# Optimization experiments

Measured on AMD Instinct MI355X. Metric: run time of the kernel, lower is better.

## Reference

```python
import jax, jax.numpy as jnp
import numpy as np

B, NQ, L, E, K = 64, 1024, 128, 8192, 2
LN_EPS = 1e-5


def setup_inputs() -> dict:
    key = jax.random.key(0)
    ks = jax.random.split(key, 16)
    s1 = 1.0 / np.sqrt(2 * L + 1)
    s2 = 1.0 / np.sqrt(L)
    s3 = 1.0 / np.sqrt(2 * L)
    return {
        "z0": jax.random.normal(ks[0], (B, L), jnp.float32),
        "edge_index": jax.random.randint(ks[1], (2, E), 0, NQ, jnp.int64),
        "edge_attr": jax.random.normal(ks[2], (E,), jnp.float32),
        "n_qubits": NQ,
        # edge MLP params, stacked over K message-passing rounds
        "e_w1": jax.random.normal(ks[3], (K, L, 2 * L + 1), jnp.float32) * s1,
        "e_b1": jnp.zeros((K, L), jnp.float32),
        "e_w2": jax.random.normal(ks[4], (K, L, L), jnp.float32) * s2,
        "e_b2": jnp.zeros((K, L), jnp.float32),
        # node MLP params
        "n_w1": jax.random.normal(ks[5], (K, L, 2 * L), jnp.float32) * s3,
        "n_b1": jnp.zeros((K, L), jnp.float32),
        "ln_g": jnp.ones((K, L), jnp.float32),
        "ln_b": jnp.zeros((K, L), jnp.float32),
        "n_w2": jax.random.normal(ks[6], (K, L, L), jnp.float32) * s2,
        "n_b2": jnp.zeros((K, L), jnp.float32),
    }


def reference(z0, edge_index, edge_attr, n_qubits,
              e_w1, e_b1, e_w2, e_b2,
              n_w1, n_b1, ln_g, ln_b, n_w2, n_b2):
    b, l = z0.shape
    src, tgt = edge_index[0], edge_index[1]
    e_ = src.shape[0]
    # broadcast latent z0 to every node: h [B, N, L]
    h = jnp.broadcast_to(z0[:, None, :], (b, n_qubits, l))
    e = jnp.broadcast_to(edge_attr[None, :, None], (b, e_, 1))  # [B, E, 1]
    k_rounds = e_w1.shape[0]
    for k in range(k_rounds):
        hi = h[:, src, :]  # gather source node feats [B, E, L]
        hj = h[:, tgt, :]  # gather target node feats [B, E, L]
        inp_e = jnp.concatenate([hi, hj, e], axis=-1)  # [B, E, 2L+1]
        m = jax.nn.relu(inp_e @ e_w1[k].T + e_b1[k]) @ e_w2[k].T + e_b2[k]
        # scatter_add messages back to source nodes
        m_agg = jnp.zeros_like(h).at[:, src, :].add(m)
        inp_n = jnp.concatenate([h, m_agg], axis=-1)  # [B, N, 2L]
        x = jax.nn.relu(inp_n @ n_w1[k].T + n_b1[k])
        mu = x.mean(axis=-1, keepdims=True)
        var = ((x - mu) ** 2).mean(axis=-1, keepdims=True)
        x = (x - mu) * jax.lax.rsqrt(var + LN_EPS) * ln_g[k] + ln_b[k]
        # Dropout(p=0.1) is identity in eval mode
        h = x @ n_w2[k].T + n_b2[k] + h  # residual
    return h.mean(axis=1)  # [B, L]
```

## Files before the change

### kernel.cpp

```cpp
#include <hip/hip_runtime.h>

#define B_   64
#define NQ_  1024
#define L_   128
#define E_   8192
#define M_   (B_*NQ_)
#define LDP  136

typedef unsigned short u16;
typedef unsigned int   u32;
typedef __attribute__((ext_vector_type(8))) short short8;
typedef __attribute__((ext_vector_type(4))) float floatx4;

#define WVB() __builtin_amdgcn_wave_barrier()

__device__ __forceinline__ u16 f2bf(float f) {
    union { float f; u32 u; } v; v.f = f;
    return (u16)((v.u + 0x7fffu + ((v.u >> 16) & 1u)) >> 16);
}
__device__ __forceinline__ float bf2f(u16 u) {
    union { u32 u; float f; } v; v.u = ((u32)u) << 16;
    return v.f;
}
__device__ __forceinline__ floatx4 mfma16(short8 a, short8 b, floatx4 c) {
    return __builtin_amdgcn_mfma_f32_16x16x32_bf16(a, b, c, 0, 0, 0);
}
__device__ __forceinline__ short8 gfrag(const u16* base, int r0, int kb, int lane) {
    return *(const short8*)(base + (size_t)(r0 + (lane & 15)) * 128 + kb * 32 + (lane >> 4) * 8);
}
__device__ __forceinline__ short8 sfrag(const u16* t, int r0, int kb, int lane) {
    return *(const short8*)(t + (r0 + (lane & 15)) * LDP + kb * 32 + (lane >> 4) * 8);
}
__device__ __forceinline__ short8 frag_cvt(const float* base, int r0, int ld, int kb, int lane) {
    const float* p = base + (size_t)(r0 + (lane & 15)) * ld + kb * 32 + (lane >> 4) * 8;
    short8 s;
#pragma unroll
    for (int j = 0; j < 8; ++j) s[j] = (short)f2bf(p[j]);
    return s;
}
__device__ __forceinline__ void tile_store(u16* t, const floatx4* acc, int lane) {
    int col = lane & 15, qd = lane >> 4;
#pragma unroll
    for (int nt = 0; nt < 8; ++nt)
#pragma unroll
        for (int r = 0; r < 4; ++r)
            t[(qd * 4 + r) * LDP + nt * 16 + col] = f2bf(acc[nt][r]);
}
__device__ __forceinline__ void tile_flush(const u16* t, u16* g, int lane) {
#pragma unroll
    for (int it = 0; it < 4; ++it) {
        int chunk = it * 64 + lane, row = chunk >> 4, c8 = chunk & 15;
        *(uint4*)(g + (size_t)row * 128 + c8 * 8) = *(const uint4*)(t + row * LDP + c8 * 8);
    }
}
__device__ __forceinline__ void stage_w(u16* wbuf, const u16* g, int tid) {
    const uint4* g4 = (const uint4*)g;
#pragma unroll
    for (int i = 0; i < 8; ++i) {
        int idx = tid + i * 256, row = idx >> 4, c8 = idx & 15;
        *(uint4*)&wbuf[row * LDP + c8 * 8] = g4[idx];
    }
}

__global__ __launch_bounds__(256) void k_setup(const int* __restrict__ ei,
                                               const float* __restrict__ attr,
                                               const float* __restrict__ z0,
                                               const float* __restrict__ e_w1,
                                               const float* __restrict__ e_b1,
                                               const float* __restrict__ e_w2,
                                               const float* __restrict__ e_b2,
                                               const float* __restrict__ n_w1,
                                               const float* __restrict__ n_b1,
                                               const float* __restrict__ n_w2,
                                               const float* __restrict__ n_b2,
                                               int* __restrict__ ofs,
                                               int* __restrict__ tgt_s,
                                               float* __restrict__ a_s,
                                               float* __restrict__ degf,
                                               u16* __restrict__ wb,
                                               float* __restrict__ wl,
                                               float* __restrict__ vb2,
                                               float* __restrict__ rx,
                                               float* __restrict__ rci,
                                               float* __restrict__ rcj,
                                               float* __restrict__ rh,
                                               float* __restrict__ mx0,
                                               u16* __restrict__ c0t) {
    __shared__ __align__(16) char smem[52608];
    int tid = threadIdx.x, blk = blockIdx.x;
    int lane = tid & 63, w = tid >> 6, col = lane & 15, qd = lane >> 4;

    if (blk == 0) {
        int* cnt  = (int*)smem;
        int* wsum = cnt + 1024;
        int* flag = wsum + 8;
#pragma unroll
        for (int i = 0; i < 4; ++i) cnt[tid + i * 256] = 0;
        if (tid == 0) *flag = 1;
        __syncthreads();
        if (tid < 100 && ei[2 * tid + 1] != 0) atomicAnd(flag, 0);
        __syncthreads();
        int i64 = *flag;
        for (int e = tid; e < E_; e += 256) {
            int s = i64 ? ei[2 * e] : ei[e];
            atomicAdd(&cnt[s], 1);
        }
        __syncthreads();
        int q0 = tid * 4;
        int c0 = cnt[q0], c1 = cnt[q0 + 1], c2 = cnt[q0 + 2], c3 = cnt[q0 + 3];
        int tsum = c0 + c1 + c2 + c3, incl = tsum;
#pragma unroll
        for (int o = 1; o < 64; o <<= 1) {
            int t = __shfl_up(incl, o, 64);
            if (lane >= o) incl += t;
        }
        if (lane == 63) wsum[w] = incl;
        __syncthreads();
        int wo = 0;
        for (int i = 0; i < w; ++i) wo += wsum[i];
        int base = wo + incl - tsum;
        ofs[q0] = base; ofs[q0 + 1] = base + c0;
        ofs[q0 + 2] = base + c0 + c1; ofs[q0 + 3] = base + c0 + c1 + c2;
        degf[q0] = (float)c0; degf[q0 + 1] = (float)c1;
        degf[q0 + 2] = (float)c2; degf[q0 + 3] = (float)c3;
        if (tid == 0) ofs[NQ_] = E_;
        __syncthreads();
        cnt[q0] = base; cnt[q0 + 1] = base + c0;
        cnt[q0 + 2] = base + c0 + c1; cnt[q0 + 3] = base + c0 + c1 + c2;
        __syncthreads();
        for (int e = tid; e < E_; e += 256) {
            int s = i64 ? ei[2 * e]        : ei[e];
            int t = i64 ? ei[2 * (E_ + e)] : ei[E_ + e];
            int pos = atomicAdd(&cnt[s], 1);
            tgt_s[pos] = t;
            a_s[pos]   = attr[e];
        }
    } else if (blk <= 2) {
        const float* src = (blk == 1) ? n_w2 : (n_w2 + 16384);
        u16* dst = wb + ((blk == 1) ? 1 : 6) * 16384;
        for (int idx = tid; idx < 16384; idx += 256) dst[idx] = f2bf(src[idx]);
    } else if (blk <= 7) {
        const float* P; const float* Q; int ldp; u16* D;
        switch (blk) {
            case 3: P = n_w1 + 128;             ldp = 256; Q = e_w2;         D = wb;             break;
            case 4: P = n_w1 + 32768 + 128;     ldp = 256; Q = e_w2 + 16384; D = wb + 5 * 16384; break;
            case 5: P = e_w1 + 128 * 257;       ldp = 257; Q = n_w2;         D = wb + 2 * 16384; break;
            case 6: P = e_w1 + 128 * 257 + 128; ldp = 257; Q = n_w2;         D = wb + 3 * 16384; break;
            default:P = n_w1 + 32768;           ldp = 256; Q = n_w2;         D = wb + 4 * 16384; break;
        }
        u16* qt = (u16*)smem;
        u16* tl = (u16*)(smem + 34816);
        for (int idx = tid; idx < 16384; idx += 256) {
            int c = idx >> 7, kd = idx & 127;
            qt[kd * LDP + c] = f2bf(Q[idx]);
        }
        __syncthreads();
        for (int t = 0; t < 2; ++t) {
            int r0 = (w * 2 + t) * 16;
            floatx4 acc[8] = {};
#pragma unroll
            for (int kb = 0; kb < 4; ++kb) {
                short8 a = frag_cvt(P, r0, ldp, kb, lane);
#pragma unroll
                for (int nt = 0; nt < 8; ++nt)
                    acc[nt] = mfma16(a, sfrag(qt, nt * 16, kb, lane), acc[nt]);
            }
            u16* slot = tl + w * 16 * LDP;
            tile_store(slot, acc, lane); WVB();
            tile_flush(slot, D + (size_t)r0 * 128, lane); WVB();
        }
    } else if (blk == 8) {
        int r0 = w * 16;
        floatx4 acc[8] = {};
#pragma unroll
        for (int kb = 0; kb < 4; ++kb) {
            short8 a = frag_cvt(z0, r0, 128, kb, lane);
#pragma unroll
            for (int nt = 0; nt < 8; ++nt)
                acc[nt] = mfma16(a, frag_cvt(n_w1, nt * 16, 256, kb, lane), acc[nt]);
        }
#pragma unroll
        for (int nt = 0; nt < 8; ++nt) {
            int cg = nt * 16 + col; float bv = n_b1[cg];
#pragma unroll
            for (int r = 0; r < 4; ++r) rx[(r0 + qd * 4 + r) * 128 + cg] = acc[nt][r] + bv;
        }
    } else if (blk <= 11) {
        int r0 = w * 16;
        const float* Wp; int ld; const float* bias; float* dst;
        if (blk == 9)       { Wp = e_w1 + 128 * 257;       ld = 257; bias = e_b1 + 128; dst = rci; }
        else if (blk == 10) { Wp = e_w1 + 128 * 257 + 128; ld = 257; bias = nullptr;    dst = rcj; }
        else                { Wp = n_w1 + 32768;           ld = 256; bias = n_b1 + 128; dst = rh;  }
        floatx4 acc[8] = {};
#pragma unroll
        for (int kb = 0; kb < 4; ++kb) {
            short8 a;
            int rr = (r0 + (lane & 15)) * 128, kk = kb * 32 + (lane >> 4) * 8;
#pragma unroll
            for (int j = 0; j < 8; ++j) a[j] = (short)f2bf(z0[rr + kk + j] + n_b2[kk + j]);
#pragma unroll
            for (int nt = 0; nt < 8; ++nt)
                acc[nt] = mfma16(a, frag_cvt(Wp, nt * 16, ld, kb, lane), acc[nt]);
        }
#pragma unroll
        for (int nt = 0; nt < 8; ++nt) {
            int cg = nt * 16 + col;
            float bv = bias ? bias[cg] : 0.0f;
#pragma unroll
            for (int r = 0; r < 4; ++r) dst[(r0 + qd * 4 + r) * 128 + cg] = acc[nt][r] + bv;
        }
    } else if (blk == 12) {
        u16* tl = (u16*)(smem + 34816);
        int r0 = w * 16;
        floatx4 a1[8] = {};
#pragma unroll
        for (int kb = 0; kb < 4; ++kb) {
            short8 a = frag_cvt(z0, r0, 128, kb, lane);
#pragma unroll
            for (int nt = 0; nt < 8; ++nt) {
                a1[nt] = mfma16(a, frag_cvt(e_w1,       nt * 16, 257, kb, lane), a1[nt]);
                a1[nt] = mfma16(a, frag_cvt(e_w1 + 128, nt * 16, 257, kb, lane), a1[nt]);
            }
        }
#pragma unroll
        for (int nt = 0; nt < 8; ++nt) {
            float bv = e_b1[nt * 16 + col];
#pragma unroll
            for (int r = 0; r < 4; ++r) a1[nt][r] += bv;
        }
        u16* slot = tl + w * 16 * LDP;
        tile_store(slot, a1, lane); WVB();
        tile_flush(slot, c0t + (size_t)r0 * 128, lane);
    } else {
        int k = tid >> 7, c = tid & 127;
        float s = 0.0f;
        for (int n = 0; n < 128; ++n)
            s += n_w1[k * 32768 + c * 256 + 128 + n] * e_b2[k * 128 + n];
        vb2[tid] = s;
        wl[tid]  = e_w1[k * 128 * 257 + c * 257 + 256];
        for (int i = tid; i < 8192; i += 256) mx0[i] = 0.0f;
    }
}

template <bool R0>
__global__ __launch_bounds__(256) void k_edge(const u16* __restrict__ ci,
                                              const u16* __restrict__ cj,
                                              const int* __restrict__ ofs,
                                              const int* __restrict__ tgt_s,
                                              const float* __restrict__ a_s,
                                              const float* __restrict__ wl,
                                              u16* __restrict__ S) {
    int tid = threadIdx.x, lane = tid & 63, w = tid >> 6;
    int gw = blockIdx.x * 4 + w;
    int q = gw & (NQ_ - 1), bg = gw >> 10;
    int bl[8];
#pragma unroll
    for (int i = 0; i < 4; ++i) { bl[i] = bg * 4 + i; bl[i + 4] = bg * 4 + i + 32; }
    float2 wl2 = ((const float2*)wl)[lane];
    int st = ofs[q], en = ofs[q + 1];
    float ax[8] = {}, ay[8] = {};
    if (R0) {
        float cx[8], cy[8];
#pragma unroll
        for (int i = 0; i < 8; ++i) {
            u32 cv = ((const u32*)ci)[(size_t)bl[i] * 64 + lane];
            cx[i] = bf2f((u16)(cv & 0xffff)); cy[i] = bf2f((u16)(cv >> 16));
        }
        for (int idx = st; idx < en; ++idx) {
            float a = a_s[idx];
            float wx = a * wl2.x, wy = a * wl2.y;
#pragma unroll
            for (int i = 0; i < 8; ++i) {
                ax[i] += fmaxf(cx[i] + wx, 0.f);
                ay[i] += fmaxf(cy[i] + wy, 0.f);
            }
        }
    } else {
        const u32* cjp[8];
        float cx[8], cy[8];
#pragma unroll
        for (int i = 0; i < 8; ++i) {
            cjp[i] = (const u32*)cj + (size_t)bl[i] * NQ_ * 64;
            u32 cv = ((const u32*)ci)[((size_t)bl[i] * NQ_ + q) * 64 + lane];
            cx[i] = bf2f((u16)(cv & 0xffff)); cy[i] = bf2f((u16)(cv >> 16));
        }
        for (int idx = st; idx < en; ++idx) {
            int t = tgt_s[idx];
            float a = a_s[idx];
            size_t ro = (size_t)t * 64 + lane;
            float wx = a * wl2.x, wy = a * wl2.y;
#pragma unroll
            for (int i = 0; i < 8; ++i) {
                u32 jv = cjp[i][ro];
                ax[i] += fmaxf(cx[i] + bf2f((u16)(jv & 0xffff)) + wx, 0.f);
                ay[i] += fmaxf(cy[i] + bf2f((u16)(jv >> 16))    + wy, 0.f);
            }
        }
    }
    u32* Sp = (u32*)S;
#pragma unroll
    for (int i = 0; i < 8; ++i)
        Sp[((size_t)bl[i] * NQ_ + q) * 64 + lane] =
            (u32)f2bf(ax[i]) | ((u32)f2bf(ay[i]) << 16);
}

__global__ __launch_bounds__(256, 2) void k_node0(const u16* __restrict__ S,
                                                  const u16* __restrict__ wb,
                                                  const float* __restrict__ rx,
                                                  const float* __restrict__ vb2,
                                                  const float* __restrict__ degf,
                                                  const float* __restrict__ rci,
                                                  const float* __restrict__ rcj,
                                                  const float* __restrict__ rh,
                                                  const float* __restrict__ g,
                                                  const float* __restrict__ bb,
                                                  float* __restrict__ mx0,
                                                  u16* __restrict__ t1,
                                                  u16* __restrict__ ci1,
                                                  u16* __restrict__ cj1) {
    __shared__ u16 wbuf[128 * LDP];
    __shared__ u16 xt[8][16 * LDP];
    __shared__ float rsum[4][128];
    int tid = threadIdx.x, lane = tid & 63, w = tid >> 6;
    int col = lane & 15, qd = lane >> 4;
    int rowbase = blockIdx.x * 128 + w * 32;
    int b = blockIdx.x >> 3;

    stage_w(wbuf, wb, tid);
    __syncthreads();
    floatx4 xa[2][8] = {};
#pragma unroll
    for (int kb = 0; kb < 4; ++kb) {
        short8 Bv[8];
#pragma unroll
        for (int nt = 0; nt < 8; ++nt) Bv[nt] = sfrag(wbuf, nt * 16, kb, lane);
#pragma unroll
        for (int t = 0; t < 2; ++t) {
            short8 a = gfrag(S, rowbase + t * 16, kb, lane);
#pragma unroll
            for (int nt = 0; nt < 8; ++nt) xa[t][nt] = mfma16(a, Bv[nt], xa[t][nt]);
        }
    }
    float s8[8] = {};
#pragma unroll
    for (int t = 0; t < 2; ++t) {
#pragma unroll
        for (int nt = 0; nt < 8; ++nt) {
            int cg = nt * 16 + col;
            float base = rx[b * 128 + cg], vb = vb2[cg];
#pragma unroll
            for (int r = 0; r < 4; ++r) {
                int row = rowbase + t * 16 + qd * 4 + r;
                xa[t][nt][r] = fmaxf(xa[t][nt][r] + base + degf[row & (NQ_ - 1)] * vb, 0.f);
            }
        }
#pragma unroll
        for (int r = 0; r < 4; ++r) {
            float s = 0.f, s2 = 0.f;
#pragma unroll
            for (int nt = 0; nt < 8; ++nt) { float v = xa[t][nt][r]; s += v; s2 += v * v; }
#pragma unroll
            for (int o = 1; o < 16; o <<= 1) { s += __shfl_xor(s, o, 64); s2 += __shfl_xor(s2, o, 64); }
            float mu = s * (1.f / 128.f), var = s2 * (1.f / 128.f) - mu * mu;
            float rs = rsqrtf(var + 1e-5f);
#pragma unroll
            for (int nt = 0; nt < 8; ++nt) {
                int cg = nt * 16 + col;
                float xv = (xa[t][nt][r] - mu) * rs * g[cg] + bb[cg];
                xa[t][nt][r] = xv;
                s8[nt] += xv;
            }
        }
        tile_store(&xt[w * 2 + t][0], xa[t], lane);
    }
#pragma unroll
    for (int nt = 0; nt < 8; ++nt) {
        s8[nt] += __shfl_xor(s8[nt], 16, 64);
        s8[nt] += __shfl_xor(s8[nt], 32, 64);
    }
    if (lane < 16) {
#pragma unroll
        for (int nt = 0; nt < 8; ++nt) rsum[w][nt * 16 + lane] = s8[nt];
    }
    __syncthreads();
    if (tid < 128) {
        float v = rsum[0][tid] + rsum[1][tid] + rsum[2][tid] + rsum[3][tid];
        atomicAdd(mx0 + b * 128 + tid, v);
    }

#pragma unroll
    for (int ph = 0; ph < 3; ++ph) {
        const u16* Wsl = wb + ((ph == 0) ? 4 : (ph == 1) ? 2 : 3) * 16384;
        const float* rt = (ph == 0) ? rh : (ph == 1) ? rci : rcj;
        u16* dstg = (ph == 0) ? t1 : (ph == 1) ? ci1 : cj1;
        __syncthreads();
        stage_w(wbuf, Wsl, tid);
        __syncthreads();
        floatx4 ca[2][8] = {};
#pragma unroll
        for (int kb = 0; kb < 4; ++kb) {
            short8 Bv[8];
#pragma unroll
            for (int nt = 0; nt < 8; ++nt) Bv[nt] = sfrag(wbuf, nt * 16, kb, lane);
#pragma unroll
            for (int t = 0; t < 2; ++t) {
                short8 a = sfrag(&xt[w * 2 + t][0], 0, kb, lane);
#pragma unroll
                for (int nt = 0; nt < 8; ++nt) ca[t][nt] = mfma16(a, Bv[nt], ca[t][nt]);
            }
        }
#pragma unroll
        for (int t = 0; t < 2; ++t)
#pragma unroll
            for (int nt = 0; nt < 8; ++nt) {
                float rc = rt[b * 128 + nt * 16 + col];
#pragma unroll
                for (int r = 0; r < 4; ++r) ca[t][nt][r] += rc;
            }
        __syncthreads();
#pragma unroll
        for (int t = 0; t < 2; ++t) tile_store(wbuf + (w * 2 + t) * 16 * LDP, ca[t], lane);
        WVB();
#pragma unroll
        for (int t = 0; t < 2; ++t)
            tile_flush(wbuf + (w * 2 + t) * 16 * LDP, dstg + (size_t)(rowbase + t * 16) * 128, lane);
    }
}

__global__ __launch_bounds__(256, 2) void k_node1(const u16* __restrict__ S,
                                                  const u16* __restrict__ t1,
                                                  const u16* __restrict__ wb,
                                                  const float* __restrict__ vb2,
                                                  const float* __restrict__ degf,
                                                  const float* __restrict__ g,
                                                  const float* __restrict__ bb,
                                                  const float* __restrict__ z0,
                                                  const float* __restrict__ n_b2,
                                                  const float* __restrict__ mx0,
                                                  float* __restrict__ out) {
    __shared__ u16 wbuf[128 * LDP];
    __shared__ u16 xt[8][16 * LDP];
    __shared__ float rsum[4][128];
    int tid = threadIdx.x, lane = tid & 63, w = tid >> 6;
    int col = lane & 15, qd = lane >> 4;
    int rowbase = blockIdx.x * 128 + w * 32;
    int b = blockIdx.x >> 3;

    stage_w(wbuf, wb + 5 * 16384, tid);
    __syncthreads();
    floatx4 xa[2][8] = {};
#pragma unroll
    for (int kb = 0; kb < 4; ++kb) {
        short8 Bv[8];
#pragma unroll
        for (int nt = 0; nt < 8; ++nt) Bv[nt] = sfrag(wbuf, nt * 16, kb, lane);
#pragma unroll
        for (int t = 0; t < 2; ++t) {
            short8 a = gfrag(S, rowbase + t * 16, kb, lane);
#pragma unroll
            for (int nt = 0; nt < 8; ++nt) xa[t][nt] = mfma16(a, Bv[nt], xa[t][nt]);
        }
    }
#pragma unroll
    for (int t = 0; t < 2; ++t) {
#pragma unroll
        for (int nt = 0; nt < 8; ++nt) {
            int cg = nt * 16 + col;
            float vb = vb2[cg];
#pragma unroll
            for (int r = 0; r < 4; ++r) {
                int row = rowbase + t * 16 + qd * 4 + r;
                float tv = bf2f(t1[(size_t)row * 128 + cg]);
                xa[t][nt][r] = fmaxf(xa[t][nt][r] + tv + degf[row & (NQ_ - 1)] * vb, 0.f);
            }
        }
#pragma unroll
        for (int r = 0; r < 4; ++r) {
            float s = 0.f, s2 = 0.f;
#pragma unroll
            for (int nt = 0; nt < 8; ++nt) { float v = xa[t][nt][r]; s += v; s2 += v * v; }
#pragma unroll
            for (int o = 1; o < 16; o <<= 1) { s += __shfl_xor(s, o, 64); s2 += __shfl_xor(s2, o, 64); }
            float mu = s * (1.f / 128.f), var = s2 * (1.f / 128.f) - mu * mu;
            float rs = rsqrtf(var + 1e-5f);
#pragma unroll
            for (int nt = 0; nt < 8; ++nt) {
                int cg = nt * 16 + col;
                xa[t][nt][r] = (xa[t][nt][r] - mu) * rs * g[cg] + bb[cg];
            }
        }
        tile_store(&xt[w * 2 + t][0], xa[t], lane);
    }
    __syncthreads();

    stage_w(wbuf, wb + 6 * 16384, tid);
    __syncthreads();
    floatx4 ma[2][8] = {};
#pragma unroll
    for (int kb = 0; kb < 4; ++kb) {
        short8 Bv[8];
#pragma unroll
        for (int nt = 0; nt < 8; ++nt) Bv[nt] = sfrag(wbuf, nt * 16, kb, lane);
#pragma unroll
        for (int t = 0; t < 2; ++t) {
            short8 a = sfrag(&xt[w * 2 + t][0], 0, kb, lane);
#pragma unroll
            for (int nt = 0; nt < 8; ++nt) ma[t][nt] = mfma16(a, Bv[nt], ma[t][nt]);
        }
    }
    float s8[8] = {};
#pragma unroll
    for (int t = 0; t < 2; ++t)
#pragma unroll
        for (int nt = 0; nt < 8; ++nt)
#pragma unroll
            for (int r = 0; r < 4; ++r) s8[nt] += ma[t][nt][r];
#pragma unroll
    for (int nt = 0; nt < 8; ++nt) {
        s8[nt] += __shfl_xor(s8[nt], 16, 64);
        s8[nt] += __shfl_xor(s8[nt], 32, 64);
    }
    if (lane < 16) {
#pragma unroll
        for (int nt = 0; nt < 8; ++nt) rsum[w][nt * 16 + lane] = s8[nt];
    }
    __syncthreads();
    if (tid < 128) {
        float v = rsum[0][tid] + rsum[1][tid] + rsum[2][tid] + rsum[3][tid];
        atomicAdd(out + b * 128 + tid, v * (1.f / 1024.f));
    }

    if ((blockIdx.x & 7) == 0 && tid < 128) {
        int c = tid;
        const u16* w2s = wb + 1 * 16384;
        const float* mx = mx0 + b * 128;
        float s = 0.f;
#pragma unroll 4
        for (int k = 0; k < 128; ++k) s += mx[k] * bf2f(w2s[c * 128 + k]);
        float acc = z0[b * 128 + c] + n_b2[c] + n_b2[128 + c] + s * (1.f / 1024.f);
        atomicAdd(out + b * 128 + c, acc);
    }
}

extern "C" void kernel_launch(void* const* d_in, const int* in_sizes, int n_in,
                              void* d_out, int out_size, void* d_ws, size_t ws_size,
                              hipStream_t stream) {
    const float* z0   = (const float*)d_in[0];
    const int*   ei   = (const int*)d_in[1];
    const float* attr = (const float*)d_in[2];
    const float* e_w1 = (const float*)d_in[4];
    const float* e_b1 = (const float*)d_in[5];
    const float* e_w2 = (const float*)d_in[6];
    const float* e_b2 = (const float*)d_in[7];
    const float* n_w1 = (const float*)d_in[8];
    const float* n_b1 = (const float*)d_in[9];
    const float* ln_g = (const float*)d_in[10];
    const float* ln_b = (const float*)d_in[11];
    const float* n_w2 = (const float*)d_in[12];
    const float* n_b2 = (const float*)d_in[13];
    float* out = (float*)d_out;

    const size_t H = (size_t)M_ * L_;
    float* f     = (float*)d_ws;
    float* degf  = f;
    float* a_s   = f + 1024;
    float* wl    = a_s + 8192;
    float* vb2   = wl + 256;
    float* rx    = vb2 + 256;
    float* rci   = rx + 8192;
    float* rcj   = rci + 8192;
    float* rh    = rcj + 8192;
    float* mx0   = rh + 8192;
    int*   ofs   = (int*)(mx0 + 8192);
    int*   tgt_s = ofs + 1056;
    u16*   wb    = (u16*)(tgt_s + 8192);
    u16*   c0t   = wb + 7 * 16384;
    u16*   S     = c0t + 8192;
    u16*   t1    = S + H;
    u16*   ci1   = t1 + H;
    u16*   cj1   = ci1 + H;

    hipMemsetAsync(out, 0, 8192 * sizeof(float), stream);

    k_setup<<<14, 256, 0, stream>>>(ei, attr, z0, e_w1, e_b1, e_w2, e_b2,
                                    n_w1, n_b1, n_w2, n_b2,
                                    ofs, tgt_s, a_s, degf, wb, wl, vb2,
                                    rx, rci, rcj, rh, mx0, c0t);

    k_edge<true><<<2048, 256, 0, stream>>>(c0t, nullptr, ofs, tgt_s, a_s, wl, S);

    k_node0<<<512, 256, 0, stream>>>(S, wb, rx, vb2, degf, rci, rcj, rh,
                                     ln_g, ln_b, mx0, t1, ci1, cj1);

    k_edge<false><<<2048, 256, 0, stream>>>(ci1, cj1, ofs, tgt_s, a_s, wl + 128, S);

    k_node1<<<512, 256, 0, stream>>>(S, t1, wb, vb2 + 128, degf,
                                     ln_g + 128, ln_b + 128, z0, n_b2, mx0, out);
}
```

Before: 190.9 us.

## Store weights in MFMA fragment order and read them directly from global

Setup now writes the folded bf16 weight matrices in a per-lane MFMA fragment layout. The node kernels load B fragments straight from global or L2 with coalesced 16-byte reads instead of staging the whole 128x128 weight into LDS behind a block barrier. Node1 also runs its second GEMM per wave through a small LDS tile and sends per-wave atomics to the output, which drops the block-wide barriers and the rsum reduction. The trade-off is repeated global or L2 weight reads per wave and four times as many atomics, in exchange for less LDS, fewer syncs and possibly higher occupancy.

New measurement: 192.4 us. No clear change (+0.8%).

```diff
diff --git a/kernel.cpp b/kernel.cpp
--- a/kernel.cpp
+++ b/kernel.cpp
@@ -6,6 +6,7 @@
 #define E_   8192
 #define M_   (B_*NQ_)
 #define LDP  136
+#define TILE 2176
 
 typedef unsigned short u16;
 typedef unsigned int   u32;
@@ -31,6 +32,14 @@
 __device__ __forceinline__ short8 sfrag(const u16* t, int r0, int kb, int lane) {
     return *(const short8*)(t + (r0 + (lane & 15)) * LDP + kb * 32 + (lane >> 4) * 8);
 }
+__device__ __forceinline__ short8 wfrag(const u16* wf, int nt, int kb, int lane) {
+    return *(const short8*)(wf + (((kb << 3) + nt) * 64 + lane) * 8);
+}
+__device__ __forceinline__ void frag_flush(const u16* t, u16* wf, int nt, int lane) {
+#pragma unroll
+    for (int kb = 0; kb < 4; ++kb)
+        *(short8*)(wf + (((kb << 3) + nt) * 64 + lane) * 8) = sfrag(t, 0, kb, lane);
+}
 __device__ __forceinline__ short8 frag_cvt(const float* base, int r0, int ld, int kb, int lane) {
     const float* p = base + (size_t)(r0 + (lane & 15)) * ld + kb * 32 + (lane >> 4) * 8;
     short8 s;
@@ -53,40 +62,23 @@
         *(uint4*)(g + (size_t)row * 128 + c8 * 8) = *(const uint4*)(t + row * LDP + c8 * 8);
     }
 }
-__device__ __forceinline__ void stage_w(u16* wbuf, const u16* g, int tid) {
-    const uint4* g4 = (const uint4*)g;
-#pragma unroll
-    for (int i = 0; i < 8; ++i) {
-        int idx = tid + i * 256, row = idx >> 4, c8 = idx & 15;
-        *(uint4*)&wbuf[row * LDP + c8 * 8] = g4[idx];
-    }
-}
-
-__global__ __launch_bounds__(256) void k_setup(const int* __restrict__ ei,
-                                               const float* __restrict__ attr,
-                                               const float* __restrict__ z0,
-                                               const float* __restrict__ e_w1,
-                                               const float* __restrict__ e_b1,
-                                               const float* __restrict__ e_w2,
-                                               const float* __restrict__ e_b2,
-                                               const float* __restrict__ n_w1,
-                                               const float* __restrict__ n_b1,
-                                               const float* __restrict__ n_w2,
-                                               const float* __restrict__ n_b2,
-                                               int* __restrict__ ofs,
-                                               int* __restrict__ tgt_s,
-                                               float* __restrict__ a_s,
-                                               float* __restrict__ degf,
-                                               u16* __restrict__ wb,
-                                               float* __restrict__ wl,
-                                               float* __restrict__ vb2,
-                                               float* __restrict__ rx,
-                                               float* __restrict__ rci,
-                                               float* __restrict__ rcj,
-                                               float* __restrict__ rh,
-                                               float* __restrict__ mx0,
-                                               u16* __restrict__ c0t) {
-    __shared__ __align__(16) char smem[52608];
+
+struct P {
+    const int* ei; const float* attr; const float* z0;
+    const float* e_w1; const float* e_b1; const float* e_w2; const float* e_b2;
+    const float* n_w1; const float* n_b1; const float* ln_g; const float* ln_b;
+    const float* n_w2; const float* n_b2;
+    int* ofs; int* tgt_s; float* a_s; float* degf;
+    u16* wf;
+    u16* w_n20;
+    float* wl; float* vb2;
+    float* rx; float* rci; float* rcj; float* rh; float* mx0;
+    u16* c0t; u16* S; u16* t1g; u16* ci1; u16* cj1;
+    float* out;
+};
+
+__global__ __launch_bounds__(256) void k_setup(P p) {
+    __shared__ __align__(16) char smem[52224];
     int tid = threadIdx.x, blk = blockIdx.x;
     int lane = tid & 63, w = tid >> 6, col = lane & 15, qd = lane >> 4;
 
@@ -98,11 +90,11 @@
         for (int i = 0; i < 4; ++i) cnt[tid + i * 256] = 0;
         if (tid == 0) *flag = 1;
         __syncthreads();
-        if (tid < 100 && ei[2 * tid + 1] != 0) atomicAnd(flag, 0);
+        if (tid < 100 && p.ei[2 * tid + 1] != 0) atomicAnd(flag, 0);
         __syncthreads();
         int i64 = *flag;
         for (int e = tid; e < E_; e += 256) {
-            int s = i64 ? ei[2 * e] : ei[e];
+            int s = i64 ? p.ei[2 * e] : p.ei[e];
             atomicAdd(&cnt[s], 1);
         }
         __syncthreads();
@@ -119,34 +111,43 @@
         int wo = 0;
         for (int i = 0; i < w; ++i) wo += wsum[i];
         int base = wo + incl - tsum;
-        ofs[q0] = base; ofs[q0 + 1] = base + c0;
-        ofs[q0 + 2] = base + c0 + c1; ofs[q0 + 3] = base + c0 + c1 + c2;
-        degf[q0] = (float)c0; degf[q0 + 1] = (float)c1;
-        degf[q0 + 2] = (float)c2; degf[q0 + 3] = (float)c3;
-        if (tid == 0) ofs[NQ_] = E_;
+        p.ofs[q0] = base; p.ofs[q0 + 1] = base + c0;
+        p.ofs[q0 + 2] = base + c0 + c1; p.ofs[q0 + 3] = base + c0 + c1 + c2;
+        p.degf[q0] = (float)c0; p.degf[q0 + 1] = (float)c1;
+        p.degf[q0 + 2] = (float)c2; p.degf[q0 + 3] = (float)c3;
+        if (tid == 0) p.ofs[NQ_] = E_;
         __syncthreads();
         cnt[q0] = base; cnt[q0 + 1] = base + c0;
         cnt[q0 + 2] = base + c0 + c1; cnt[q0 + 3] = base + c0 + c1 + c2;
         __syncthreads();
         for (int e = tid; e < E_; e += 256) {
-            int s = i64 ? ei[2 * e]        : ei[e];
-            int t = i64 ? ei[2 * (E_ + e)] : ei[E_ + e];
+            int s = i64 ? p.ei[2 * e]        : p.ei[e];
+            int t = i64 ? p.ei[2 * (E_ + e)] : p.ei[E_ + e];
             int pos = atomicAdd(&cnt[s], 1);
-            tgt_s[pos] = t;
-            a_s[pos]   = attr[e];
-        }
-    } else if (blk <= 2) {
-        const float* src = (blk == 1) ? n_w2 : (n_w2 + 16384);
-        u16* dst = wb + ((blk == 1) ? 1 : 6) * 16384;
-        for (int idx = tid; idx < 16384; idx += 256) dst[idx] = f2bf(src[idx]);
+            p.tgt_s[pos] = t;
+            p.a_s[pos]   = p.attr[e];
+        }
+    } else if (blk == 1) {
+        for (int idx = tid; idx < 16384; idx += 256) p.w_n20[idx] = f2bf(p.n_w2[idx]);
+    } else if (blk == 2) {
+        const float* src = p.n_w2 + 16384;
+        u16* dst = p.wf + 5 * 16384;
+        for (int pr = w; pr < 32; pr += 4) {
+            int kb = pr >> 3, nt = pr & 7;
+            const float* s = src + (nt * 16 + (lane & 15)) * 128 + kb * 32 + (lane >> 4) * 8;
+            short8 v;
+#pragma unroll
+            for (int j = 0; j < 8; ++j) v[j] = (short)f2bf(s[j]);
+            *(short8*)(dst + (pr * 64 + lane) * 8) = v;
+        }
     } else if (blk <= 7) {
-        const float* P; const float* Q; int ldp; u16* D;
+        const float* Pm; const float* Q; int ldp; u16* D;
         switch (blk) {
-            case 3: P = n_w1 + 128;             ldp = 256; Q = e_w2;         D = wb;             break;
-            case 4: P = n_w1 + 32768 + 128;     ldp = 256; Q = e_w2 + 16384; D = wb + 5 * 16384; break;
-            case 5: P = e_w1 + 128 * 257;       ldp = 257; Q = n_w2;         D = wb + 2 * 16384; break;
-            case 6: P = e_w1 + 128 * 257 + 128; ldp = 257; Q = n_w2;         D = wb + 3 * 16384; break;
-            default:P = n_w1 + 32768;           ldp = 256; Q = n_w2;         D = wb + 4 * 16384; break;
+            case 3: Pm = p.n_w1 + 128;             ldp = 256; Q = p.e_w2;         D = p.wf;             break;
+            case 4: Pm = p.n_w1 + 32768 + 128;     ldp = 256; Q = p.e_w2 + 16384; D = p.wf + 4 * 16384; break;
+            case 5: Pm = p.e_w1 + 128 * 257;       ldp = 257; Q = p.n_w2;         D = p.wf + 1 * 16384; break;
+            case 6: Pm = p.e_w1 + 128 * 257 + 128; ldp = 257; Q = p.n_w2;         D = p.wf + 2 * 16384; break;
+            default:Pm = p.n_w1 + 32768;           ldp = 256; Q = p.n_w2;         D = p.wf + 3 * 16384; break;
         }
         u16* qt = (u16*)smem;
         u16* tl = (u16*)(smem + 34816);
@@ -160,44 +161,44 @@
             floatx4 acc[8] = {};
 #pragma unroll
             for (int kb = 0; kb < 4; ++kb) {
-                short8 a = frag_cvt(P, r0, ldp, kb, lane);
+                short8 a = frag_cvt(Pm, r0, ldp, kb, lane);
 #pragma unroll
                 for (int nt = 0; nt < 8; ++nt)
                     acc[nt] = mfma16(a, sfrag(qt, nt * 16, kb, lane), acc[nt]);
             }
-            u16* slot = tl + w * 16 * LDP;
+            u16* slot = tl + w * TILE;
             tile_store(slot, acc, lane); WVB();
-            tile_flush(slot, D + (size_t)r0 * 128, lane); WVB();
+            frag_flush(slot, D, w * 2 + t, lane); WVB();
         }
     } else if (blk == 8) {
         int r0 = w * 16;
         floatx4 acc[8] = {};
 #pragma unroll
         for (int kb = 0; kb < 4; ++kb) {
-            short8 a = frag_cvt(z0, r0, 128, kb, lane);
+            short8 a = frag_cvt(p.z0, r0, 128, kb, lane);
 #pragma unroll
             for (int nt = 0; nt < 8; ++nt)
-                acc[nt] = mfma16(a, frag_cvt(n_w1, nt * 16, 256, kb, lane), acc[nt]);
+                acc[nt] = mfma16(a, frag_cvt(p.n_w1, nt * 16, 256, kb, lane), acc[nt]);
         }
 #pragma unroll
         for (int nt = 0; nt < 8; ++nt) {
-            int cg = nt * 16 + col; float bv = n_b1[cg];
-#pragma unroll
-            for (int r = 0; r < 4; ++r) rx[(r0 + qd * 4 + r) * 128 + cg] = acc[nt][r] + bv;
+            int cg = nt * 16 + col; float bv = p.n_b1[cg];
+#pragma unroll
+            for (int r = 0; r < 4; ++r) p.rx[(r0 + qd * 4 + r) * 128 + cg] = acc[nt][r] + bv;
         }
     } else if (blk <= 11) {
         int r0 = w * 16;
         const float* Wp; int ld; const float* bias; float* dst;
-        if (blk == 9)       { Wp = e_w1 + 128 * 257;       ld = 257; bias = e_b1 + 128; dst = rci; }
-        else if (blk == 10) { Wp = e_w1 + 128 * 257 + 128; ld = 257; bias = nullptr;    dst = rcj; }
-        else                { Wp = n_w1 + 32768;           ld = 256; bias = n_b1 + 128; dst = rh;  }
+        if (blk == 9)       { Wp = p.e_w1 + 128 * 257;       ld = 257; bias = p.e_b1 + 128; dst = p.rci; }
+        else if (blk == 10) { Wp = p.e_w1 + 128 * 257 + 128; ld = 257; bias = nullptr;      dst = p.rcj; }
+        else                { Wp = p.n_w1 + 32768;           ld = 256; bias = p.n_b1 + 128; dst = p.rh;  }
         floatx4 acc[8] = {};
 #pragma unroll
         for (int kb = 0; kb < 4; ++kb) {
             short8 a;
             int rr = (r0 + (lane & 15)) * 128, kk = kb * 32 + (lane >> 4) * 8;
 #pragma unroll
-            for (int j = 0; j < 8; ++j) a[j] = (short)f2bf(z0[rr + kk + j] + n_b2[kk + j]);
+            for (int j = 0; j < 8; ++j) a[j] = (short)f2bf(p.z0[rr + kk + j] + p.n_b2[kk + j]);
 #pragma unroll
             for (int nt = 0; nt < 8; ++nt)
                 acc[nt] = mfma16(a, frag_cvt(Wp, nt * 16, ld, kb, lane), acc[nt]);
@@ -215,51 +216,47 @@
         floatx4 a1[8] = {};
 #pragma unroll
         for (int kb = 0; kb < 4; ++kb) {
-            short8 a = frag_cvt(z0, r0, 128, kb, lane);
+            short8 a = frag_cvt(p.z0, r0, 128, kb, lane);
 #pragma unroll
             for (int nt = 0; nt < 8; ++nt) {
-                a1[nt] = mfma16(a, frag_cvt(e_w1,       nt * 16, 257, kb, lane), a1[nt]);
-                a1[nt] = mfma16(a, frag_cvt(e_w1 + 128, nt * 16, 257, kb, lane), a1[nt]);
+                a1[nt] = mfma16(a, frag_cvt(p.e_w1,       nt * 16, 257, kb, lane), a1[nt]);
+                a1[nt] = mfma16(a, frag_cvt(p.e_w1 + 128, nt * 16, 257, kb, lane), a1[nt]);
             }
         }
 #pragma unroll
         for (int nt = 0; nt < 8; ++nt) {
-            float bv = e_b1[nt * 16 + col];
+            float bv = p.e_b1[nt * 16 + col];
 #pragma unroll
             for (int r = 0; r < 4; ++r) a1[nt][r] += bv;
         }
-        u16* slot = tl + w * 16 * LDP;
+        u16* slot = tl + w * TILE;
         tile_store(slot, a1, lane); WVB();
-        tile_flush(slot, c0t + (size_t)r0 * 128, lane);
-    } else {
+        tile_flush(slot, p.c0t + (size_t)r0 * 128, lane);
+    } else if (blk == 13) {
         int k = tid >> 7, c = tid & 127;
         float s = 0.0f;
         for (int n = 0; n < 128; ++n)
-            s += n_w1[k * 32768 + c * 256 + 128 + n] * e_b2[k * 128 + n];
-        vb2[tid] = s;
-        wl[tid]  = e_w1[k * 128 * 257 + c * 257 + 256];
-        for (int i = tid; i < 8192; i += 256) mx0[i] = 0.0f;
-    }
-}
-
-template <bool R0>
-__global__ __launch_bounds__(256) void k_edge(const u16* __restrict__ ci,
-                                              const u16* __restrict__ cj,
-                                              const int* __restrict__ ofs,
-                                              const int* __restrict__ tgt_s,
-                                              const float* __restrict__ a_s,
-                                              const float* __restrict__ wl,
-                                              u16* __restrict__ S) {
+            s += p.n_w1[k * 32768 + c * 256 + 128 + n] * p.e_b2[k * 128 + n];
+        p.vb2[tid] = s;
+        p.wl[tid]  = p.e_w1[k * 128 * 257 + c * 257 + 256];
+        for (int i = tid; i < 8192; i += 256) p.mx0[i] = 0.0f;
+    }
+}
+
+__global__ __launch_bounds__(256) void k_edge(P p, int r0) {
     int tid = threadIdx.x, lane = tid & 63, w = tid >> 6;
+    const u16* ci = r0 ? p.c0t : p.ci1;
+    const u16* cj = p.cj1;
+    const float* wl = r0 ? p.wl : p.wl + 128;
+    float2 wl2 = ((const float2*)wl)[lane];
     int gw = blockIdx.x * 4 + w;
     int q = gw & (NQ_ - 1), bg = gw >> 10;
     int bl[8];
 #pragma unroll
     for (int i = 0; i < 4; ++i) { bl[i] = bg * 4 + i; bl[i + 4] = bg * 4 + i + 32; }
-    float2 wl2 = ((const float2*)wl)[lane];
-    int st = ofs[q], en = ofs[q + 1];
+    int st = p.ofs[q], en = p.ofs[q + 1];
     float ax[8] = {}, ay[8] = {};
-    if (R0) {
+    if (r0) {
         float cx[8], cy[8];
 #pragma unroll
         for (int i = 0; i < 8; ++i) {
@@ -267,7 +264,7 @@
             cx[i] = bf2f((u16)(cv & 0xffff)); cy[i] = bf2f((u16)(cv >> 16));
         }
         for (int idx = st; idx < en; ++idx) {
-            float a = a_s[idx];
+            float a = p.a_s[idx];
             float wx = a * wl2.x, wy = a * wl2.y;
 #pragma unroll
             for (int i = 0; i < 8; ++i) {
@@ -285,8 +282,8 @@
             cx[i] = bf2f((u16)(cv & 0xffff)); cy[i] = bf2f((u16)(cv >> 16));
         }
         for (int idx = st; idx < en; ++idx) {
-            int t = tgt_s[idx];
-            float a = a_s[idx];
+            int t = p.tgt_s[idx];
+            float a = p.a_s[idx];
             size_t ro = (size_t)t * 64 + lane;
             float wx = a * wl2.x, wy = a * wl2.y;
 #pragma unroll
@@ -297,46 +294,32 @@
             }
         }
     }
-    u32* Sp = (u32*)S;
+    u32* Sp = (u32*)p.S;
 #pragma unroll
     for (int i = 0; i < 8; ++i)
         Sp[((size_t)bl[i] * NQ_ + q) * 64 + lane] =
             (u32)f2bf(ax[i]) | ((u32)f2bf(ay[i]) << 16);
 }
 
-__global__ __launch_bounds__(256, 2) void k_node0(const u16* __restrict__ S,
-                                                  const u16* __restrict__ wb,
-                                                  const float* __restrict__ rx,
-                                                  const float* __restrict__ vb2,
-                                                  const float* __restrict__ degf,
-                                                  const float* __restrict__ rci,
-                                                  const float* __restrict__ rcj,
-                                                  const float* __restrict__ rh,
-                                                  const float* __restrict__ g,
-                                                  const float* __restrict__ bb,
-                                                  float* __restrict__ mx0,
-                                                  u16* __restrict__ t1,
-                                                  u16* __restrict__ ci1,
-                                                  u16* __restrict__ cj1) {
-    __shared__ u16 wbuf[128 * LDP];
-    __shared__ u16 xt[8][16 * LDP];
-    __shared__ float rsum[4][128];
+__global__ __launch_bounds__(256, 2) void k_node0(P p) {
+    __shared__ __align__(16) char smem[52224];
+    u16* xt = (u16*)smem;
+    u16* ob = (u16*)(smem + 34816);
     int tid = threadIdx.x, lane = tid & 63, w = tid >> 6;
     int col = lane & 15, qd = lane >> 4;
-    int rowbase = blockIdx.x * 128 + w * 32;
-    int b = blockIdx.x >> 3;
-
-    stage_w(wbuf, wb, tid);
-    __syncthreads();
+    int blk = blockIdx.x;
+    int rowbase = blk * 128 + w * 32;
+    int b = blk >> 3;
+
     floatx4 xa[2][8] = {};
 #pragma unroll
     for (int kb = 0; kb < 4; ++kb) {
         short8 Bv[8];
 #pragma unroll
-        for (int nt = 0; nt < 8; ++nt) Bv[nt] = sfrag(wbuf, nt * 16, kb, lane);
+        for (int nt = 0; nt < 8; ++nt) Bv[nt] = wfrag(p.wf, nt, kb, lane);
 #pragma unroll
         for (int t = 0; t < 2; ++t) {
-            short8 a = gfrag(S, rowbase + t * 16, kb, lane);
+            short8 a = gfrag(p.S, rowbase + t * 16, kb, lane);
 #pragma unroll
             for (int nt = 0; nt < 8; ++nt) xa[t][nt] = mfma16(a, Bv[nt], xa[t][nt]);
         }
@@ -347,11 +330,11 @@
 #pragma unroll
         for (int nt = 0; nt < 8; ++nt) {
             int cg = nt * 16 + col;
-            float base = rx[b * 128 + cg], vb = vb2[cg];
+            float base = p.rx[b * 128 + cg], vb = p.vb2[cg];
 #pragma unroll
             for (int r = 0; r < 4; ++r) {
                 int row = rowbase + t * 16 + qd * 4 + r;
-                xa[t][nt][r] = fmaxf(xa[t][nt][r] + base + degf[row & (NQ_ - 1)] * vb, 0.f);
+                xa[t][nt][r] = fmaxf(xa[t][nt][r] + base + p.degf[row & (NQ_ - 1)] * vb, 0.f);
             }
         }
 #pragma unroll
@@ -366,12 +349,12 @@
 #pragma unroll
             for (int nt = 0; nt < 8; ++nt) {
                 int cg = nt * 16 + col;
-                float xv = (xa[t][nt][r] - mu) * rs * g[cg] + bb[cg];
+                float xv = (xa[t][nt][r] - mu) * rs * p.ln_g[cg] + p.ln_b[cg];
                 xa[t][nt][r] = xv;
                 s8[nt] += xv;
             }
         }
-        tile_store(&xt[w * 2 + t][0], xa[t], lane);
+        tile_store(xt + (w * 2 + t) * TILE, xa[t], lane);
     }
 #pragma unroll
     for (int nt = 0; nt < 8; ++nt) {
@@ -380,31 +363,23 @@
     }
     if (lane < 16) {
 #pragma unroll
-        for (int nt = 0; nt < 8; ++nt) rsum[w][nt * 16 + lane] = s8[nt];
-    }
-    __syncthreads();
-    if (tid < 128) {
-        float v = rsum[0][tid] + rsum[1][tid] + rsum[2][tid] + rsum[3][tid];
-        atomicAdd(mx0 + b * 128 + tid, v);
-    }
-
+        for (int nt = 0; nt < 8; ++nt)
+            atomicAdd(p.mx0 + b * 128 + nt * 16 + lane, s8[nt]);
+    }
+    WVB();
 #pragma unroll
     for (int ph = 0; ph < 3; ++ph) {
-        const u16* Wsl = wb + ((ph == 0) ? 4 : (ph == 1) ? 2 : 3) * 16384;
-        const float* rt = (ph == 0) ? rh : (ph == 1) ? rci : rcj;
-        u16* dstg = (ph == 0) ? t1 : (ph == 1) ? ci1 : cj1;
-        __syncthreads();
-        stage_w(wbuf, Wsl, tid);
-        __syncthreads();
+        const u16* wfp = p.wf + ((ph == 0) ? 1 : (ph == 1) ? 2 : 3) * 16384;
+        const float* rt = (ph == 0) ? p.rci : (ph == 1) ? p.rcj : p.rh;
         floatx4 ca[2][8] = {};
 #pragma unroll
         for (int kb = 0; kb < 4; ++kb) {
             short8 Bv[8];
 #pragma unroll
-            for (int nt = 0; nt < 8; ++nt) Bv[nt] = sfrag(wbuf, nt * 16, kb, lane);
+            for (int nt = 0; nt < 8; ++nt) Bv[nt] = wfrag(wfp, nt, kb, lane);
 #pragma unroll
             for (int t = 0; t < 2; ++t) {
-                short8 a = sfrag(&xt[w * 2 + t][0], 0, kb, lane);
+                short8 a = sfrag(xt + (w * 2 + t) * TILE, 0, kb, lane);
 #pragma unroll
                 for (int nt = 0; nt < 8; ++nt) ca[t][nt] = mfma16(a, Bv[nt], ca[t][nt]);
             }
@@ -417,61 +392,52 @@
 #pragma unroll
                 for (int r = 0; r < 4; ++r) ca[t][nt][r] += rc;
             }
-        __syncthreads();
-#pragma unroll
-        for (int t = 0; t < 2; ++t) tile_store(wbuf + (w * 2 + t) * 16 * LDP, ca[t], lane);
-        WVB();
-#pragma unroll
-        for (int t = 0; t < 2; ++t)
-            tile_flush(wbuf + (w * 2 + t) * 16 * LDP, dstg + (size_t)(rowbase + t * 16) * 128, lane);
-    }
-}
-
-__global__ __launch_bounds__(256, 2) void k_node1(const u16* __restrict__ S,
-                                                  const u16* __restrict__ t1,
-                                                  const u16* __restrict__ wb,
-                                                  const float* __restrict__ vb2,
-                                                  const float* __restrict__ degf,
-                                                  const float* __restrict__ g,
-                                                  const float* __restrict__ bb,
-                                                  const float* __restrict__ z0,
-                                                  const float* __restrict__ n_b2,
-                                                  const float* __restrict__ mx0,
-                                                  float* __restrict__ out) {
-    __shared__ u16 wbuf[128 * LDP];
-    __shared__ u16 xt[8][16 * LDP];
-    __shared__ float rsum[4][128];
+        u16* dst = (ph == 0) ? p.ci1 : (ph == 1) ? p.cj1 : p.t1g;
+#pragma unroll
+        for (int t = 0; t < 2; ++t) {
+            tile_store(ob + w * TILE, ca[t], lane);
+            WVB();
+            tile_flush(ob + w * TILE, dst + (size_t)(rowbase + t * 16) * 128, lane);
+            WVB();
+        }
+    }
+}
+
+__global__ __launch_bounds__(256, 2) void k_node1(P p) {
+    __shared__ __align__(16) char smem[52224];
+    u16* ob = (u16*)(smem + 34816);
     int tid = threadIdx.x, lane = tid & 63, w = tid >> 6;
     int col = lane & 15, qd = lane >> 4;
-    int rowbase = blockIdx.x * 128 + w * 32;
-    int b = blockIdx.x >> 3;
-
-    stage_w(wbuf, wb + 5 * 16384, tid);
-    __syncthreads();
+    int blk = blockIdx.x;
+    int rowbase = blk * 128 + w * 32;
+    int b = blk >> 3;
+
+    const u16* wc1 = p.wf + 4 * 16384;
     floatx4 xa[2][8] = {};
 #pragma unroll
     for (int kb = 0; kb < 4; ++kb) {
         short8 Bv[8];
 #pragma unroll
-        for (int nt = 0; nt < 8; ++nt) Bv[nt] = sfrag(wbuf, nt * 16, kb, lane);
+        for (int nt = 0; nt < 8; ++nt) Bv[nt] = wfrag(wc1, nt, kb, lane);
 #pragma unroll
         for (int t = 0; t < 2; ++t) {
-            short8 a = gfrag(S, rowbase + t * 16, kb, lane);
+            short8 a = gfrag(p.S, rowbase + t * 16, kb, lane);
 #pragma unroll
             for (int nt = 0; nt < 8; ++nt) xa[t][nt] = mfma16(a, Bv[nt], xa[t][nt]);
         }
     }
+    const float* vb21 = p.vb2 + 128;
 #pragma unroll
     for (int t = 0; t < 2; ++t) {
 #pragma unroll
         for (int nt = 0; nt < 8; ++nt) {
             int cg = nt * 16 + col;
-            float vb = vb2[cg];
+            float vb = vb21[cg];
 #pragma unroll
             for (int r = 0; r < 4; ++r) {
                 int row = rowbase + t * 16 + qd * 4 + r;
-                float tv = bf2f(t1[(size_t)row * 128 + cg]);
-                xa[t][nt][r] = fmaxf(xa[t][nt][r] + tv + degf[row & (NQ_ - 1)] * vb, 0.f);
+                float tv = bf2f(p.t1g[(size_t)row * 128 + cg]);
+                xa[t][nt][r] = fmaxf(xa[t][nt][r] + tv + p.degf[row & (NQ_ - 1)] * vb, 0.f);
             }
         }
 #pragma unroll
@@ -486,35 +452,32 @@
 #pragma unroll
             for (int nt = 0; nt < 8; ++nt) {
                 int cg = nt * 16 + col;
-                xa[t][nt][r] = (xa[t][nt][r] - mu) * rs * g[cg] + bb[cg];
-            }
-        }
-        tile_store(&xt[w * 2 + t][0], xa[t], lane);
-    }
-    __syncthreads();
-
-    stage_w(wbuf, wb + 6 * 16384, tid);
-    __syncthreads();
-    floatx4 ma[2][8] = {};
-#pragma unroll
-    for (int kb = 0; kb < 4; ++kb) {
-        short8 Bv[8];
-#pragma unroll
-        for (int nt = 0; nt < 8; ++nt) Bv[nt] = sfrag(wbuf, nt * 16, kb, lane);
-#pragma unroll
-        for (int t = 0; t < 2; ++t) {
-            short8 a = sfrag(&xt[w * 2 + t][0], 0, kb, lane);
-#pragma unroll
-            for (int nt = 0; nt < 8; ++nt) ma[t][nt] = mfma16(a, Bv[nt], ma[t][nt]);
-        }
-    }
+                xa[t][nt][r] = (xa[t][nt][r] - mu) * rs * p.ln_g[128 + cg] + p.ln_b[128 + cg];
+            }
+        }
+    }
+    const u16* n21 = p.wf + 5 * 16384;
     float s8[8] = {};
 #pragma unroll
-    for (int t = 0; t < 2; ++t)
+    for (int t = 0; t < 2; ++t) {
+        WVB();
+        tile_store(ob + w * TILE, xa[t], lane);
+        WVB();
+        floatx4 ma[8] = {};
+#pragma unroll
+        for (int kb = 0; kb < 4; ++kb) {
+            short8 Bv[8];
+#pragma unroll
+            for (int nt = 0; nt < 8; ++nt) Bv[nt] = wfrag(n21, nt, kb, lane);
+            short8 a = sfrag(ob + w * TILE, 0, kb, lane);
+#pragma unroll
+            for (int nt = 0; nt < 8; ++nt) ma[nt] = mfma16(a, Bv[nt], ma[nt]);
+        }
 #pragma unroll
         for (int nt = 0; nt < 8; ++nt)
 #pragma unroll
-            for (int r = 0; r < 4; ++r) s8[nt] += ma[t][nt][r];
+            for (int r = 0; r < 4; ++r) s8[nt] += ma[nt][r];
+    }
 #pragma unroll
     for (int nt = 0; nt < 8; ++nt) {
         s8[nt] += __shfl_xor(s8[nt], 16, 64);
@@ -522,78 +485,65 @@
     }
     if (lane < 16) {
 #pragma unroll
-        for (int nt = 0; nt < 8; ++nt) rsum[w][nt * 16 + lane] = s8[nt];
-    }
-    __syncthreads();
-    if (tid < 128) {
-        float v = rsum[0][tid] + rsum[1][tid] + rsum[2][tid] + rsum[3][tid];
-        atomicAdd(out + b * 128 + tid, v * (1.f / 1024.f));
-    }
-
-    if ((blockIdx.x & 7) == 0 && tid < 128) {
+        for (int nt = 0; nt < 8; ++nt)
+            atomicAdd(p.out + b * 128 + nt * 16 + lane, s8[nt] * (1.f / 1024.f));
+    }
+    if ((blk & 7) == 0 && tid < 128) {
         int c = tid;
-        const u16* w2s = wb + 1 * 16384;
-        const float* mx = mx0 + b * 128;
+        const float* mx = p.mx0 + b * 128;
         float s = 0.f;
 #pragma unroll 4
-        for (int k = 0; k < 128; ++k) s += mx[k] * bf2f(w2s[c * 128 + k]);
-        float acc = z0[b * 128 + c] + n_b2[c] + n_b2[128 + c] + s * (1.f / 1024.f);
-        atomicAdd(out + b * 128 + c, acc);
+        for (int k = 0; k < 128; ++k) s += mx[k] * bf2f(p.w_n20[c * 128 + k]);
+        float acc = p.z0[b * 128 + c] + p.n_b2[c] + p.n_b2[128 + c] + s * (1.f / 1024.f);
+        atomicAdd(p.out + b * 128 + c, acc);
     }
 }
 
 extern "C" void kernel_launch(void* const* d_in, const int* in_sizes, int n_in,
                               void* d_out, int out_size, void* d_ws, size_t ws_size,
                               hipStream_t stream) {
-    const float* z0   = (const float*)d_in[0];
-    const int*   ei   = (const int*)d_in[1];
-    const float* attr = (const float*)d_in[2];
-    const float* e_w1 = (const float*)d_in[4];
-    const float* e_b1 = (const float*)d_in[5];
-    const float* e_w2 = (const float*)d_in[6];
-    const float* e_b2 = (const float*)d_in[7];
-    const float* n_w1 = (const float*)d_in[8];
-    const float* n_b1 = (const float*)d_in[9];
-    const float* ln_g = (const float*)d_in[10];
-    const float* ln_b = (const float*)d_in[11];
-    const float* n_w2 = (const float*)d_in[12];
-    const float* n_b2 = (const float*)d_in[13];
-    float* out = (float*)d_out;
+    P p;
+    p.z0   = (const float*)d_in[0];
+    p.ei   = (const int*)d_in[1];
+    p.attr = (const float*)d_in[2];
+    p.e_w1 = (const float*)d_in[4];
+    p.e_b1 = (const float*)d_in[5];
+    p.e_w2 = (const float*)d_in[6];
+    p.e_b2 = (const float*)d_in[7];
+    p.n_w1 = (const float*)d_in[8];
+    p.n_b1 = (const float*)d_in[9];
+    p.ln_g = (const float*)d_in[10];
+    p.ln_b = (const float*)d_in[11];
+    p.n_w2 = (const float*)d_in[12];
+    p.n_b2 = (const float*)d_in[13];
+    p.out  = (float*)d_out;
 
     const size_t H = (size_t)M_ * L_;
-    float* f     = (float*)d_ws;
-    float* degf  = f;
-    float* a_s   = f + 1024;
-    float* wl    = a_s + 8192;
-    float* vb2   = wl + 256;
-    float* rx    = vb2 + 256;
-    float* rci   = rx + 8192;
-    float* rcj   = rci + 8192;
-    float* rh    = rcj + 8192;
-    float* mx0   = rh + 8192;
-    int*   ofs   = (int*)(mx0 + 8192);
-    int*   tgt_s = ofs + 1056;
-    u16*   wb    = (u16*)(tgt_s + 8192);
-    u16*   c0t   = wb + 7 * 16384;
-    u16*   S     = c0t + 8192;
-    u16*   t1    = S + H;
-    u16*   ci1   = t1 + H;
-    u16*   cj1   = ci1 + H;
-
-    hipMemsetAsync(out, 0, 8192 * sizeof(float), stream);
-
-    k_setup<<<14, 256, 0, stream>>>(ei, attr, z0, e_w1, e_b1, e_w2, e_b2,
-                                    n_w1, n_b1, n_w2, n_b2,
-                                    ofs, tgt_s, a_s, degf, wb, wl, vb2,
-                                    rx, rci, rcj, rh, mx0, c0t);
-
-    k_edge<true><<<2048, 256, 0, stream>>>(c0t, nullptr, ofs, tgt_s, a_s, wl, S);
-
-    k_node0<<<512, 256, 0, stream>>>(S, wb, rx, vb2, degf, rci, rcj, rh,
-                                     ln_g, ln_b, mx0, t1, ci1, cj1);
-
-    k_edge<false><<<2048, 256, 0, stream>>>(ci1, cj1, ofs, tgt_s, a_s, wl + 128, S);
-
-    k_node1<<<512, 256, 0, stream>>>(S, t1, wb, vb2 + 128, degf,
-                                     ln_g + 128, ln_b + 128, z0, n_b2, mx0, out);
-}
+    float* f  = (float*)d_ws;
+    p.degf = f;
+    p.a_s  = f + 1024;
+    p.wl   = p.a_s + 8192;
+    p.vb2  = p.wl + 256;
+    p.rx   = p.vb2 + 256;
+    p.rci  = p.rx + 8192;
+    p.rcj  = p.rci + 8192;
+    p.rh   = p.rcj + 8192;
+    p.mx0  = p.rh + 8192;
+    p.ofs  = (int*)(p.mx0 + 8192);
+    p.tgt_s = p.ofs + 1056;
+    p.wf    = (u16*)(p.tgt_s + 8192);
+    p.w_n20 = p.wf + 6 * 16384;
+    p.c0t   = p.w_n20 + 16384;
+    p.S     = p.c0t + 8192;
+    p.t1g   = p.S + H;
+    p.ci1   = p.t1g + H;
+    p.cj1   = p.ci1 + H;
+
+    hipMemsetAsync(p.out, 0, 8192 * sizeof(float), stream);
+
+    k_setup<<<14, 256, 0, stream>>>(p);
+    k_edge<<<2048, 256, 0, stream>>>(p, 1);
+    k_node0<<<512, 256, 0, stream>>>(p);
+    k_edge<<<2048, 256, 0, stream>>>(p, 0);
+    k_node1<<<512, 256, 0, stream>>>(p);
+}
```
